# Kernel tuning notes

Measured on AMD Instinct MI355X. Metric: run time of the kernel, lower is better.

## Reference

```python
import jax, jax.numpy as jnp
import numpy as np

VOCAB, EMBED, HIDDEN = 32000, 512, 1024
B, T = 8, 256

def setup_inputs() -> dict:
    key = jax.random.key(0)
    ks = jax.random.split(key, 5)
    x = jax.random.randint(ks[0], (B, T), 0, VOCAB)
    embedding = jax.random.normal(ks[1], (VOCAB, EMBED), dtype=jnp.float32)
    W_xh = jax.random.normal(ks[2], (EMBED, HIDDEN), dtype=jnp.float32) * 0.01
    W_hh = jax.random.normal(ks[3], (HIDDEN, HIDDEN), dtype=jnp.float32) * 0.01
    b_h = jnp.zeros((HIDDEN,), dtype=jnp.float32)
    W_hy = jax.random.normal(ks[4], (HIDDEN, VOCAB), dtype=jnp.float32) * 0.01
    b_y = jnp.zeros((VOCAB,), dtype=jnp.float32)
    return {"x": x, "embedding": embedding, "W_xh": W_xh, "W_hh": W_hh,
            "b_h": b_h, "W_hy": W_hy, "b_y": b_y}

def reference(x, embedding, W_xh, W_hh, b_h, W_hy, b_y):
    # x: [B,T] int ids
    emb = embedding[x]                      # [B,T,E]
    # Precompute input contribution for all steps: [B,T,H]
    xh = jnp.einsum('bte,eh->bth', emb, W_xh) + b_h
    h0 = jnp.zeros((x.shape[0], W_hh.shape[0]), dtype=emb.dtype)

    def step(h, xh_t):
        h = jnp.tanh(xh_t + h @ W_hh)       # [B,H]
        return h, h

    _, hs = jax.lax.scan(step, h0, jnp.swapaxes(xh, 0, 1))  # hs: [T,B,H]
    hs = jnp.swapaxes(hs, 0, 1)             # [B,T,H]
    # Output projection batched over all timesteps (same math as per-step)
    y = jnp.einsum('bth,hv->btv', hs, W_hy) + b_y  # [B,T,V]
    return y
```

## Files before the change

kernel.cpp:

```cpp
#include <hip/hip_runtime.h>
#include <hip/hip_bf16.h>

#define VOCAB 32000
#define EMBED 512
#define HIDDEN 1024
#define NB 8
#define NT 256
#define XH_ROWS 16

#define NCH 8
#define NMEM 32
#define RCOLS 32
#define NBLK_REC 256
#define NBLK_TR 64
#define TILES_PER_TR 500

typedef __attribute__((ext_vector_type(8))) short bf16x8;
typedef __attribute__((ext_vector_type(4))) float f32x4;
typedef __attribute__((ext_vector_type(4))) unsigned u32x4;

#define AS1 __attribute__((address_space(1)))
#define AS3 __attribute__((address_space(3)))

__device__ __forceinline__ unsigned short bf16_bits(float f) {
    __hip_bfloat16 b = __float2bfloat16(f);
    unsigned short s;
    __builtin_memcpy(&s, &b, 2);
    return s;
}
__device__ __forceinline__ float lo16f(unsigned u) { return __uint_as_float(u << 16); }
__device__ __forceinline__ float hi16f(unsigned u) { return __uint_as_float(u & 0xffff0000u); }

__global__ __launch_bounds__(256) void k_xh(const int* __restrict__ ids,
                                            const float* __restrict__ emb,
                                            const float* __restrict__ Wxh,
                                            const float* __restrict__ bh,
                                            float* __restrict__ xh) {
    __shared__ alignas(16) float embS[XH_ROWS][EMBED];
    __shared__ int idsS[XH_ROWS];
    const int tid = threadIdx.x;
    const int blk = blockIdx.x;
    if (tid < XH_ROWS) idsS[tid] = ids[blk * XH_ROWS + tid];
    __syncthreads();
    const float4* emb4 = (const float4*)emb;
#pragma unroll
    for (int rep = 0; rep < (XH_ROWS * EMBED / 4) / 256; ++rep) {
        const int lin = rep * 256 + tid;
        const int r = lin >> 7;
        const int e4 = lin & 127;
        *(float4*)&embS[r][e4 * 4] = emb4[(size_t)idsS[r] * (EMBED / 4) + e4];
    }
    __syncthreads();
    float4 acc[XH_ROWS] = {};
    const float4* W4 = (const float4*)Wxh;
    for (int e = 0; e < EMBED; ++e) {
        const float4 w = W4[(size_t)e * (HIDDEN / 4) + tid];
#pragma unroll
        for (int r = 0; r < XH_ROWS; ++r) {
            const float ev = embS[r][e];
            acc[r].x += ev * w.x; acc[r].y += ev * w.y;
            acc[r].z += ev * w.z; acc[r].w += ev * w.w;
        }
    }
    const float4 bv = ((const float4*)bh)[tid];
#pragma unroll
    for (int r = 0; r < XH_ROWS; ++r) {
        float4 o;
        o.x = acc[r].x + bv.x; o.y = acc[r].y + bv.y;
        o.z = acc[r].z + bv.z; o.w = acc[r].w + bv.w;
        ((float4*)xh)[(size_t)(blk * XH_ROWS + r) * (HIDDEN / 4) + tid] = o;
    }
}

__global__ __launch_bounds__(256, 1) void k_fused(const float* __restrict__ Whh,
                                                  const float* __restrict__ xh,
                                                  unsigned long long* __restrict__ hx,
                                                  __hip_bfloat16* __restrict__ hs,
                                                  const float* __restrict__ Why,
                                                  __hip_bfloat16* __restrict__ Wt) {
    __shared__ float xhS[NT * RCOLS];
    __shared__ float hS[16 * 68];
    __shared__ float red[16 * 33];
    const int tid = threadIdx.x;
    const int bid = blockIdx.x;

    if (bid >= NBLK_REC) {
        const int tb = bid - NBLK_REC;
        float (*tile)[33] = (float(*)[33])xhS;
        const int cc = tid & 31;
        const int r0 = tid >> 5;
        for (int i = 0; i < TILES_PER_TR; ++i) {
            const int g = tb * TILES_PER_TR + i;
            const int n0 = (g % 1000) * 32;
            const int k0 = (g / 1000) * 32;
            __syncthreads();
#pragma unroll
            for (int rr = 0; rr < 4; ++rr) {
                const int r = r0 + rr * 8;
                tile[cc][r] = Why[(size_t)(k0 + r) * VOCAB + n0 + cc];
            }
            __syncthreads();
#pragma unroll
            for (int rr = 0; rr < 4; ++rr) {
                const int n = r0 + rr * 8;
                Wt[(size_t)(n0 + n) * HIDDEN + k0 + cc] = __float2bfloat16(tile[n][cc]);
            }
        }
        return;
    }

    const int c = bid & (NCH - 1);
    const int m = bid >> 3;
    const int j0 = m * RCOLS;
    unsigned long long* hxc = hx + (size_t)c * 1024;

    if (tid < 16)
        __hip_atomic_store(&hxc[512 + m * 16 + tid], 0ull, __ATOMIC_RELAXED,
                           __HIP_MEMORY_SCOPE_AGENT);

    const int col2 = tid & 15;
    const int part = tid >> 4;

    u32x4 wreg[16];
#pragma unroll
    for (int j = 0; j < 16; ++j) {
        u32x4 q;
#pragma unroll
        for (int e = 0; e < 4; ++e) {
            const int i = part * 64 + 4 * j + e;
            const float2 wv = *(const float2*)&Whh[(size_t)i * HIDDEN + j0 + 2 * col2];
            q[e] = (unsigned)bf16_bits(wv.x) | ((unsigned)bf16_bits(wv.y) << 16);
        }
        wreg[j] = q;
    }
    for (int idx = tid; idx < NT * RCOLS; idx += 256) {
        const int t = idx >> 5;
        const int col = idx & 31;
        xhS[idx] = xh[(size_t)(c * NT + t) * HIDDEN + j0 + col];
    }
    __syncthreads();

    const f32x4* hv4 = (const f32x4*)&hS[part * 68];
    const int w0 = tid;
    const int w1 = tid + 256;
    const int pe0 = 2 * tid + 4 * (tid >> 5);

    for (int t = 0; t < NT; ++t) {
        unsigned long long* rbuf = hxc + ((t + 1) & 1) * 512;
        unsigned long long* wbuf = hxc + (t & 1) * 512;
        const unsigned long long tok = (unsigned long long)(unsigned)t;
        unsigned long long a = __hip_atomic_load(&rbuf[w0], __ATOMIC_RELAXED, __HIP_MEMORY_SCOPE_AGENT);
        unsigned long long b = __hip_atomic_load(&rbuf[w1], __ATOMIC_RELAXED, __HIP_MEMORY_SCOPE_AGENT);
        while (((a & 0xffffull) != tok) | ((b & 0xffffull) != tok)) {
            __builtin_amdgcn_s_sleep(1);
            if ((a & 0xffffull) != tok)
                a = __hip_atomic_load(&rbuf[w0], __ATOMIC_RELAXED, __HIP_MEMORY_SCOPE_AGENT);
            if ((b & 0xffffull) != tok)
                b = __hip_atomic_load(&rbuf[w1], __ATOMIC_RELAXED, __HIP_MEMORY_SCOPE_AGENT);
        }
        *(float2*)&hS[pe0] = make_float2(__uint_as_float(((unsigned)(a >> 16) & 0xffffu) << 16),
                                         __uint_as_float(((unsigned)(a >> 32) & 0xffffu) << 16));
        *(float2*)&hS[pe0 + 544] = make_float2(__uint_as_float(((unsigned)(b >> 16) & 0xffffu) << 16),
                                               __uint_as_float(((unsigned)(b >> 32) & 0xffffu) << 16));
        __syncthreads();
        float a0 = 0.f, a1 = 0.f;
#pragma unroll
        for (int j = 0; j < 16; ++j) {
            const u32x4 w4 = wreg[j];
            const f32x4 h4 = hv4[j];
            a0 = fmaf(lo16f(w4.x), h4.x, a0); a1 = fmaf(hi16f(w4.x), h4.x, a1);
            a0 = fmaf(lo16f(w4.y), h4.y, a0); a1 = fmaf(hi16f(w4.y), h4.y, a1);
            a0 = fmaf(lo16f(w4.z), h4.z, a0); a1 = fmaf(hi16f(w4.z), h4.z, a1);
            a0 = fmaf(lo16f(w4.w), h4.w, a0); a1 = fmaf(hi16f(w4.w), h4.w, a1);
        }
        red[part * 33 + 2 * col2]     = a0;
        red[part * 33 + 2 * col2 + 1] = a1;
        __syncthreads();
        if (tid < RCOLS) {
            float s = 0.f;
#pragma unroll
            for (int p = 0; p < 16; ++p) s += red[p * 33 + tid];
            const float v = tanhf(xhS[t * RCOLS + tid] + s);
            const unsigned hb = (unsigned)bf16_bits(v);
            ((unsigned short*)hs)[(size_t)(c * NT + t) * HIDDEN + j0 + tid] = (unsigned short)hb;
            const unsigned pb = (unsigned)__shfl_xor((int)hb, 1, 64);
            if ((tid & 1) == 0) {
                const unsigned long long wv = (unsigned long long)(unsigned)(t + 1)
                                            | ((unsigned long long)hb << 16)
                                            | ((unsigned long long)pb << 32);
                __hip_atomic_store(&wbuf[m * 16 + (tid >> 1)], wv, __ATOMIC_RELAXED,
                                   __HIP_MEMORY_SCOPE_AGENT);
            }
        }
    }
}

__global__ __launch_bounds__(512, 2) void k_proj(const unsigned short* __restrict__ A,
                                                 const unsigned short* __restrict__ Bt,
                                                 const float* __restrict__ by,
                                                 float* __restrict__ C) {
    __shared__ unsigned short LDS[4][16384];
    const int tid = threadIdx.x;
    const int wid = tid >> 6;
    const int lane = tid & 63;
    const int lin = blockIdx.x;
    const int swz = (lin & 7) * 125 + (lin >> 3);
    const int mt = swz & 7, nt = swz >> 3;
    const int m0 = mt * 256, n0 = nt * 256;
    const int wr = wid >> 2, wc = wid & 3;
    const int fr = lane & 15, fq = lane >> 4;
    const int srow = tid >> 3;
    const int sslot = tid & 7;

    f32x4 acc[8][4] = {};

#define STAGE(kt, bf)                                                                     \
    {                                                                                     \
        const unsigned short* Ag = A + (size_t)m0 * HIDDEN + (size_t)(kt) * 64;           \
        const unsigned short* Bg = Bt + (size_t)n0 * HIDDEN + (size_t)(kt) * 64;          \
        _Pragma("unroll")                                                                 \
        for (int j = 0; j < 4; ++j) {                                                     \
            const int r = j * 64 + srow;                                                  \
            const int ls = ((sslot ^ (r & 7)) * 8);                                       \
            __builtin_amdgcn_global_load_lds(                                             \
                (const AS1 unsigned*)(Ag + (size_t)r * HIDDEN + ls),                      \
                (AS3 unsigned*)(&LDS[(bf) * 2 + 0][j * 4096 + wid * 512]), 16, 0, 0);     \
        }                                                                                 \
        _Pragma("unroll")                                                                 \
        for (int j = 0; j < 4; ++j) {                                                     \
            const int r = j * 64 + srow;                                                  \
            const int ls = ((sslot ^ (r & 7)) * 8);                                       \
            __builtin_amdgcn_global_load_lds(                                             \
                (const AS1 unsigned*)(Bg + (size_t)r * HIDDEN + ls),                      \
                (AS3 unsigned*)(&LDS[(bf) * 2 + 1][j * 4096 + wid * 512]), 16, 0, 0);     \
        }                                                                                 \
    }

    STAGE(0, 0);
    STAGE(1, 1);

    int cur = 0;
    for (int kt = 0; kt < 16; ++kt) {
        if (kt < 15) { asm volatile("s_waitcnt vmcnt(8)" ::: "memory"); }
        else         { asm volatile("s_waitcnt vmcnt(0)" ::: "memory"); }
        __builtin_amdgcn_s_barrier();

        const unsigned short* Ab = &LDS[cur * 2 + 0][0];
        const unsigned short* Bb = &LDS[cur * 2 + 1][0];
        bf16x8 af[8][2], bg[4][2];
#pragma unroll
        for (int mi = 0; mi < 8; ++mi) {
            const int ra = wr * 128 + mi * 16 + fr;
#pragma unroll
            for (int ks = 0; ks < 2; ++ks)
                af[mi][ks] = *(const bf16x8*)&Ab[ra * 64 + (((ks * 4 + fq) ^ (fr & 7)) * 8)];
        }
#pragma unroll
        for (int ni = 0; ni < 4; ++ni) {
            const int rb = wc * 64 + ni * 16 + fr;
#pragma unroll
            for (int ks = 0; ks < 2; ++ks)
                bg[ni][ks] = *(const bf16x8*)&Bb[rb * 64 + (((ks * 4 + fq) ^ (fr & 7)) * 8)];
        }
        asm volatile("s_waitcnt lgkmcnt(0)" ::: "memory");
        __builtin_amdgcn_sched_barrier(0);
        __builtin_amdgcn_s_barrier();

        if (kt < 14) STAGE(kt + 2, cur);

        __builtin_amdgcn_s_setprio(1);
#pragma unroll
        for (int mi = 0; mi < 8; ++mi)
#pragma unroll
            for (int ni = 0; ni < 4; ++ni) {
                acc[mi][ni] = __builtin_amdgcn_mfma_f32_16x16x32_bf16(af[mi][0], bg[ni][0], acc[mi][ni], 0, 0, 0);
                acc[mi][ni] = __builtin_amdgcn_mfma_f32_16x16x32_bf16(af[mi][1], bg[ni][1], acc[mi][ni], 0, 0, 0);
            }
        __builtin_amdgcn_s_setprio(0);
        cur ^= 1;
    }
#undef STAGE

#pragma unroll
    for (int ni = 0; ni < 4; ++ni) {
        const int col = n0 + wc * 64 + ni * 16 + fr;
        const float bias = by[col];
#pragma unroll
        for (int mi = 0; mi < 8; ++mi) {
            const int row = m0 + wr * 128 + mi * 16 + fq * 4;
            float* cp = C + (size_t)row * VOCAB + col;
            cp[0]                 = acc[mi][ni][0] + bias;
            cp[(size_t)VOCAB]     = acc[mi][ni][1] + bias;
            cp[(size_t)2 * VOCAB] = acc[mi][ni][2] + bias;
            cp[(size_t)3 * VOCAB] = acc[mi][ni][3] + bias;
        }
    }
}

extern "C" void kernel_launch(void* const* d_in, const int* in_sizes, int n_in,
                              void* d_out, int out_size, void* d_ws, size_t ws_size,
                              hipStream_t stream) {
    const int*   x   = (const int*)d_in[0];
    const float* emb = (const float*)d_in[1];
    const float* Wxh = (const float*)d_in[2];
    const float* Whh = (const float*)d_in[3];
    const float* bh  = (const float*)d_in[4];
    const float* Why = (const float*)d_in[5];
    const float* by  = (const float*)d_in[6];
    float* y = (float*)d_out;

    char* ws = (char*)d_ws;
    const size_t off_xh = 0;
    const size_t off_hx = off_xh + (size_t)NB * NT * HIDDEN * 4;
    const size_t off_hs = off_hx + (size_t)NCH * 2 * 512 * 8;
    const size_t off_wt = off_hs + (size_t)NB * NT * HIDDEN * 2;
    const size_t need   = off_wt + (size_t)VOCAB * HIDDEN * 2;
    if (ws_size < need) return;

    float* xh = (float*)(ws + off_xh);
    unsigned long long* hx = (unsigned long long*)(ws + off_hx);
    __hip_bfloat16* hs = (__hip_bfloat16*)(ws + off_hs);
    __hip_bfloat16* Wt = (__hip_bfloat16*)(ws + off_wt);

    k_xh<<<dim3((NB * NT) / XH_ROWS), 256, 0, stream>>>(x, emb, Wxh, bh, xh);
    k_fused<<<dim3(NBLK_REC + NBLK_TR), 256, 0, stream>>>(Whh, xh, hx, hs, Why, Wt);
    k_proj<<<dim3((2048 / 256) * (VOCAB / 256)), 512, 0, stream>>>((const unsigned short*)hs,
                                                                   (const unsigned short*)Wt, by, y);
}
```

Before: 798.8 us.

## Batch transpose tiles in LDS and overlap GEMM LDS reads with MFMA

The W_hy transpose blocks are doubled in count, and each block now stages 8 tiles in shared memory per round so more global loads are in flight between barriers. Shared arrays are merged into one buffer to hold these tiles. In the output GEMM, the LDS fragment reads are split by k-half: the first-half MFMAs start after a partial lgkmcnt wait while the second-half reads are still outstanding. This hides LDS latency behind MFMA work, at the cost of extra transpose blocks competing with the recurrent blocks and more complex wait accounting.

```diff
diff --git a/kernel.cpp b/kernel.cpp
--- a/kernel.cpp
+++ b/kernel.cpp
@@ -12,8 +12,8 @@
 #define NMEM 32
 #define RCOLS 32
 #define NBLK_REC 256
-#define NBLK_TR 64
-#define TILES_PER_TR 500
+#define NBLK_TR 128
+#define TILES_PER_TR 250
 
 typedef __attribute__((ext_vector_type(8))) short bf16x8;
 typedef __attribute__((ext_vector_type(4))) float f32x4;
@@ -78,32 +78,51 @@
                                                   __hip_bfloat16* __restrict__ hs,
                                                   const float* __restrict__ Why,
                                                   __hip_bfloat16* __restrict__ Wt) {
-    __shared__ float xhS[NT * RCOLS];
-    __shared__ float hS[16 * 68];
-    __shared__ float red[16 * 33];
+    __shared__ alignas(16) float smemF[9808];
+    float* xhS = smemF;
+    float* hS  = smemF + 8192;
+    float* red = smemF + 9280;
     const int tid = threadIdx.x;
     const int bid = blockIdx.x;
 
     if (bid >= NBLK_REC) {
         const int tb = bid - NBLK_REC;
-        float (*tile)[33] = (float(*)[33])xhS;
         const int cc = tid & 31;
         const int r0 = tid >> 5;
-        for (int i = 0; i < TILES_PER_TR; ++i) {
-            const int g = tb * TILES_PER_TR + i;
-            const int n0 = (g % 1000) * 32;
-            const int k0 = (g / 1000) * 32;
+        const int tbase = tb * TILES_PER_TR;
+        for (int rnd = 0; rnd < (TILES_PER_TR + 7) / 8; ++rnd) {
+            const int base = rnd * 8;
             __syncthreads();
 #pragma unroll
-            for (int rr = 0; rr < 4; ++rr) {
-                const int r = r0 + rr * 8;
-                tile[cc][r] = Why[(size_t)(k0 + r) * VOCAB + n0 + cc];
+            for (int u = 0; u < 8; ++u) {
+                const int i = base + u;
+                if (i < TILES_PER_TR) {
+                    const int g = tbase + i;
+                    const int n0 = (g % 1000) * 32;
+                    const int k0 = (g / 1000) * 32;
+                    float* tile = smemF + u * 1056;
+#pragma unroll
+                    for (int rr = 0; rr < 4; ++rr) {
+                        const int r = r0 + rr * 8;
+                        tile[cc * 33 + r] = Why[(size_t)(k0 + r) * VOCAB + n0 + cc];
+                    }
+                }
             }
             __syncthreads();
 #pragma unroll
-            for (int rr = 0; rr < 4; ++rr) {
-                const int n = r0 + rr * 8;
-                Wt[(size_t)(n0 + n) * HIDDEN + k0 + cc] = __float2bfloat16(tile[n][cc]);
+            for (int u = 0; u < 8; ++u) {
+                const int i = base + u;
+                if (i < TILES_PER_TR) {
+                    const int g = tbase + i;
+                    const int n0 = (g % 1000) * 32;
+                    const int k0 = (g / 1000) * 32;
+                    float* tile = smemF + u * 1056;
+#pragma unroll
+                    for (int rr = 0; rr < 4; ++rr) {
+                        const int n = r0 + rr * 8;
+                        Wt[(size_t)(n0 + n) * HIDDEN + k0 + cc] = __float2bfloat16(tile[n * 33 + cc]);
+                    }
+                }
             }
         }
         return;
@@ -251,17 +270,32 @@
 #pragma unroll
         for (int mi = 0; mi < 8; ++mi) {
             const int ra = wr * 128 + mi * 16 + fr;
-#pragma unroll
-            for (int ks = 0; ks < 2; ++ks)
-                af[mi][ks] = *(const bf16x8*)&Ab[ra * 64 + (((ks * 4 + fq) ^ (fr & 7)) * 8)];
+            af[mi][0] = *(const bf16x8*)&Ab[ra * 64 + (((0 * 4 + fq) ^ (fr & 7)) * 8)];
         }
 #pragma unroll
         for (int ni = 0; ni < 4; ++ni) {
             const int rb = wc * 64 + ni * 16 + fr;
-#pragma unroll
-            for (int ks = 0; ks < 2; ++ks)
-                bg[ni][ks] = *(const bf16x8*)&Bb[rb * 64 + (((ks * 4 + fq) ^ (fr & 7)) * 8)];
-        }
+            bg[ni][0] = *(const bf16x8*)&Bb[rb * 64 + (((0 * 4 + fq) ^ (fr & 7)) * 8)];
+        }
+#pragma unroll
+        for (int mi = 0; mi < 8; ++mi) {
+            const int ra = wr * 128 + mi * 16 + fr;
+            af[mi][1] = *(const bf16x8*)&Ab[ra * 64 + (((1 * 4 + fq) ^ (fr & 7)) * 8)];
+        }
+#pragma unroll
+        for (int ni = 0; ni < 4; ++ni) {
+            const int rb = wc * 64 + ni * 16 + fr;
+            bg[ni][1] = *(const bf16x8*)&Bb[rb * 64 + (((1 * 4 + fq) ^ (fr & 7)) * 8)];
+        }
+        asm volatile("s_waitcnt lgkmcnt(12)" ::: "memory");
+        __builtin_amdgcn_sched_barrier(0);
+        __builtin_amdgcn_s_setprio(1);
+#pragma unroll
+        for (int mi = 0; mi < 8; ++mi)
+#pragma unroll
+            for (int ni = 0; ni < 4; ++ni)
+                acc[mi][ni] = __builtin_amdgcn_mfma_f32_16x16x32_bf16(af[mi][0], bg[ni][0], acc[mi][ni], 0, 0, 0);
+        __builtin_amdgcn_s_setprio(0);
         asm volatile("s_waitcnt lgkmcnt(0)" ::: "memory");
         __builtin_amdgcn_sched_barrier(0);
         __builtin_amdgcn_s_barrier();
@@ -272,10 +306,8 @@
 #pragma unroll
         for (int mi = 0; mi < 8; ++mi)
 #pragma unroll
-            for (int ni = 0; ni < 4; ++ni) {
-                acc[mi][ni] = __builtin_amdgcn_mfma_f32_16x16x32_bf16(af[mi][0], bg[ni][0], acc[mi][ni], 0, 0, 0);
+            for (int ni = 0; ni < 4; ++ni)
                 acc[mi][ni] = __builtin_amdgcn_mfma_f32_16x16x32_bf16(af[mi][1], bg[ni][1], acc[mi][ni], 0, 0, 0);
-            }
         __builtin_amdgcn_s_setprio(0);
         cur ^= 1;
     }
```

New measurement: 793.4 us. No clear change (-0.7%).
